# Optimization experiments

Measured on AMD Instinct MI355X. Metric: run time of the kernel, lower is better.

## Reference

```python
import jax, jax.numpy as jnp
import numpy as np

PRED_STEPS = 5
NEG = 16
C = 256
B = 64
H = 16
W = 16
SKIP = 1
EPS = 1e-11


def setup_inputs() -> dict:
    key = jax.random.key(0)
    ks = jax.random.split(key, 3 + PRED_STEPS)
    inp = {
        "z": jax.random.normal(ks[0], (B, C, H, W), jnp.float32),
        "c": jax.random.normal(ks[1], (B, C, H, W), jnp.float32),
        "Wk": jax.random.normal(ks[2], (PRED_STEPS, C, C), jnp.float32) * 0.05,
    }
    for k in range(1, PRED_STEPS + 1):
        rows = (H - k - SKIP) * W * B
        inp[f"rand_idx_{k}"] = jax.random.randint(ks[2 + k], (rows * NEG,), 0, rows, dtype=jnp.int64 if jax.config.jax_enable_x64 else jnp.int32)
    return inp


def reference(z, c, Wk, rand_idx_1, rand_idx_2, rand_idx_3, rand_idx_4, rand_idx_5):
    idx_list = [rand_idx_1, rand_idx_2, rand_idx_3, rand_idx_4, rand_idx_5]
    total_loss = jnp.float32(0.0)
    patchwise_loss = jnp.zeros((B, H, W), jnp.float32)
    patchwise_count = jnp.zeros((H, W), jnp.float32)
    for k in range(1, PRED_STEPS + 1):
        off = k + SKIP
        Hk = H - off
        # 1x1 conv projection, permuted to [Hk, W, B, C]
        ztwk = jnp.einsum('oi,bihw->hwbo', Wk[k - 1], z[:, :, off:, :])
        # random-gather negatives: [Hk, W, B, NEG, C]
        flat = ztwk.reshape(Hk * W * B, C)
        ztwk_shuf = flat[idx_list[k - 1]].reshape(Hk, W, B, NEG, C)
        # context: [Hk, W, B, C]
        ctx = jnp.transpose(c[:, :, :Hk, :], (2, 3, 0, 1))
        # scoring
        main = jnp.einsum('hwbc,hwbc->hwb', ctx, ztwk)[..., None]        # [Hk,W,B,1]
        negs = jnp.einsum('hwbc,hwbnc->hwbn', ctx, ztwk_shuf)            # [Hk,W,B,NEG]
        logits = jnp.concatenate([main, negs], axis=-1)                  # [Hk,W,B,1+NEG]
        log_fk = jnp.transpose(logits, (2, 3, 0, 1))                     # [B,1+NEG,Hk,W]
        sm = jax.nn.softmax(log_fk, axis=1)
        stu_loss = -jnp.log(sm[:, 0, :, :] + EPS)                        # [B,Hk,W]
        total_loss = total_loss + stu_loss.mean()
        patchwise_loss = patchwise_loss.at[:, off:, :].add(stu_loss)
        patchwise_loss = patchwise_loss.at[:, :H - off, :].add(stu_loss)
        ones = jnp.ones((Hk, W), jnp.float32)
        patchwise_count = patchwise_count.at[off:, :].add(ones)
        patchwise_count = patchwise_count.at[:H - off, :].add(ones)
    total_loss = total_loss / PRED_STEPS
    return (total_loss, patchwise_loss, patchwise_count)
```

## Files before the change

kernel.cpp:

```cpp
#include <hip/hip_runtime.h>
#include <hip/hip_bf16.h>
#include <math.h>

#define NEG_ 16
#define PRED_ 5
#define EPS_ 1e-11f
#define LDW 18
#define GSTR 272
#define ASTR 72

typedef __attribute__((ext_vector_type(8))) short bf16x8;
typedef __attribute__((ext_vector_type(4))) float f32x4;

static __device__ __forceinline__ unsigned short f2bu(float f) {
  __hip_bfloat16 h = __float2bfloat16(f);
  return *(unsigned short*)&h;
}


__global__ __launch_bounds__(256) void prep_all(
    const float* __restrict__ z, const float* __restrict__ c,
    const float* __restrict__ Wk,
    unsigned short* __restrict__ Zp, unsigned short* __restrict__ Cb,
    unsigned short* __restrict__ Wb) {
  __shared__ float tile[32][33];
  int tx = threadIdx.x, ty = threadIdx.y;
  if (blockIdx.y == 7) {
    if (blockIdx.z == 0 && blockIdx.x < 320) {
      int i = blockIdx.x * 256 + ty * 32 + tx;
      float4 v = ((const float4*)Wk)[i];
      ushort4 o;
      o.x = f2bu(v.x); o.y = f2bu(v.y); o.z = f2bu(v.z); o.w = f2bu(v.w);
      ((ushort4*)Wb)[i] = o;
    }
    return;
  }
  const float* in = blockIdx.z ? c : z;
  unsigned short* out = blockIdx.z ? Cb : Zp;
  int p0 = blockIdx.x * 32;
  int q0 = blockIdx.y * 32 + (blockIdx.z ? 0 : 32);
#pragma unroll
  for (int r = 0; r < 32; r += 8)
    tile[ty + r][tx] = in[(size_t)(p0 + ty + r) * 256 + q0 + tx];
  __syncthreads();
#pragma unroll
  for (int r = 0; r < 32; r += 8)
    out[(size_t)(q0 + ty + r) * 16384 + p0 + tx] = f2bu(tile[tx][ty + r]);
}

__global__ __launch_bounds__(256) void gemm_all(
    const unsigned short* __restrict__ Zp, const unsigned short* __restrict__ Wb,
    unsigned short* __restrict__ Yb) {
  const int kk = blockIdx.z;
  const int Mk = (14 - kk) * 1024;
  const int m0b = blockIdx.y * 128;
  if (m0b >= Mk) return;
  const unsigned short* A = Zp + (size_t)(kk + 2) * 1024 * 256;
  const unsigned short* Wm = Wb + (size_t)kk * 65536;
  unsigned short* Y = Yb + (size_t)kk * 14336 * 256;
  __shared__ unsigned short As[128 * ASTR];
  __shared__ unsigned short Bs[128 * ASTR];
  const int t = threadIdx.x;
  const int wid = t >> 6, lane = t & 63;
  const int wm = wid >> 1, wn = wid & 1;
  const int l15 = lane & 15, quad = lane >> 4;
  const int n0 = blockIdx.x * 128;
  const int srow = t >> 1, shalf = t & 1;
  const unsigned short* ga = A + (size_t)(m0b + srow) * 256 + shalf * 32;
  const unsigned short* gb = Wm + (size_t)(n0 + srow) * 256 + shalf * 32;
  unsigned short* wa = As + srow * ASTR + shalf * 32;
  unsigned short* wb = Bs + srow * ASTR + shalf * 32;
  f32x4 acc[4][4] = {};
  bf16x8 ra[4], rb[4];
#pragma unroll
  for (int cs = 0; cs < 4; ++cs) {
    ra[cs] = *(const bf16x8*)(ga + cs * 8);
    rb[cs] = *(const bf16x8*)(gb + cs * 8);
  }
#pragma unroll
  for (int ki = 0; ki < 4; ++ki) {
    __syncthreads();
#pragma unroll
    for (int cs = 0; cs < 4; ++cs) {
      *(bf16x8*)(wa + cs * 8) = ra[cs];
      *(bf16x8*)(wb + cs * 8) = rb[cs];
    }
    __syncthreads();
    if (ki < 3) {
      const int k1 = (ki + 1) * 64;
#pragma unroll
      for (int cs = 0; cs < 4; ++cs) {
        ra[cs] = *(const bf16x8*)(ga + k1 + cs * 8);
        rb[cs] = *(const bf16x8*)(gb + k1 + cs * 8);
      }
    }
#pragma unroll
    for (int ks = 0; ks < 2; ++ks) {
      bf16x8 af[4], bf[4];
#pragma unroll
      for (int tm = 0; tm < 4; ++tm)
        af[tm] = *(const bf16x8*)(As + (wm * 64 + tm * 16 + l15) * ASTR + ks * 32 + quad * 8);
#pragma unroll
      for (int tn = 0; tn < 4; ++tn)
        bf[tn] = *(const bf16x8*)(Bs + (wn * 64 + tn * 16 + l15) * ASTR + ks * 32 + quad * 8);
#pragma unroll
      for (int tm = 0; tm < 4; ++tm)
#pragma unroll
        for (int tn = 0; tn < 4; ++tn)
          acc[tm][tn] = __builtin_amdgcn_mfma_f32_16x16x32_bf16(
              af[tm], bf[tn], acc[tm][tn], 0, 0, 0);
    }
  }
#pragma unroll
  for (int tm = 0; tm < 4; ++tm)
#pragma unroll
    for (int tn = 0; tn < 4; ++tn)
#pragma unroll
      for (int r = 0; r < 4; ++r)
        Y[(size_t)(m0b + wm * 64 + tm * 16 + quad * 4 + r) * 256 +
          n0 + wn * 64 + tn * 16 + l15] = f2bu(acc[tm][tn][r]);
}

__global__ __launch_bounds__(256) void score_all(
    const unsigned short* __restrict__ Yb, const unsigned short* __restrict__ Cb,
    const int* __restrict__ r1, const int* __restrict__ r2,
    const int* __restrict__ r3, const int* __restrict__ r4,
    const int* __restrict__ r5, float* __restrict__ Lk) {
  __shared__ __align__(16) unsigned short gbuf[4][16 * GSTR];
  __shared__ float L[16 * LDW];
  const int wv = threadIdx.x >> 6, lane = threadIdx.x & 63;
  const int gid = blockIdx.x;
  int kk, base;
  if (gid < 896)       { kk = 0; base = 0; }
  else if (gid < 1728) { kk = 1; base = 896; }
  else if (gid < 2496) { kk = 2; base = 1728; }
  else if (gid < 3200) { kk = 3; base = 2496; }
  else                 { kk = 4; base = 3200; }
  const int Mk = (14 - kk) * 1024;
  const int m0 = (gid - base) * 16;
  const int* ridx = kk == 0 ? r1 : kk == 1 ? r2 : kk == 2 ? r3 : kk == 3 ? r4 : r5;
  const unsigned short* Y = Yb + (size_t)kk * 14336 * 256;
  const int l15 = lane & 15, quad = lane >> 4;
  const int half = lane >> 5, ch = lane & 31;
  unsigned short* mybuf = gbuf[wv];

  auto gather = [&](const unsigned short* src, int iv, bf16x8* dst) {
#pragma unroll
    for (int j = 0; j < 8; ++j) {
      int rlo = __shfl(iv, 2 * j);
      int rhi = __shfl(iv, 2 * j + 1);
      int row = half ? rhi : rlo;
      dst[j] = *(const bf16x8*)(src + (size_t)row * 256 + ch * 8);
    }
  };
  auto stage = [&](const bf16x8* g) {
#pragma unroll
    for (int j2 = 0; j2 < 8; ++j2)
      *(bf16x8*)(mybuf + (2 * j2 + half) * GSTR + ch * 8) = g[j2];
  };

  bf16x8 af[8];
  {
    bf16x8 g[8];
    gather(Cb, m0 + l15, g);
    stage(g);
#pragma unroll
    for (int tv = 0; tv < 8; ++tv)
      af[tv] = *(const bf16x8*)(mybuf + l15 * GSTR + quad * 8 + tv * 32);
  }

  const int c0 = (wv == 0) ? 0 : (4 * wv + 1);
  const int nc = (wv == 0) ? 5 : 4;
  auto load_iv = [&](int c) -> int {
    if (c == 0) return m0 + l15;
    int idx = ridx[(m0 + (c - 1)) * NEG_ + l15];
    return idx < 0 ? 0 : (idx >= Mk ? Mk - 1 : idx);
  };

  bf16x8 g[8], gn[8];
  gather(Y, load_iv(c0), g);
  for (int j = 0; j < nc; ++j) {
    if (j + 1 < nc) gather(Y, load_iv(c0 + j + 1), gn);
    stage(g);
    f32x4 acc = {};
#pragma unroll
    for (int tv = 0; tv < 8; ++tv) {
      bf16x8 bf = *(const bf16x8*)(mybuf + l15 * GSTR + quad * 8 + tv * 32);
      acc = __builtin_amdgcn_mfma_f32_16x16x32_bf16(af[tv], bf, acc, 0, 0, 0);
    }
    const int c = c0 + j;
    if (c == 0) {
#pragma unroll
      for (int r = 0; r < 4; ++r)
        if (l15 == quad * 4 + r) L[(quad * 4 + r) * LDW] = acc[r];
    } else {
      const int i = c - 1;
      if (quad == (i >> 2)) L[i * LDW + 1 + l15] = acc[i & 3];
    }
#pragma unroll
    for (int tv = 0; tv < 8; ++tv) g[tv] = gn[tv];
  }
  __syncthreads();
  if (threadIdx.x < 16) {
    float mainv = L[threadIdx.x * LDW];
    float mx = mainv;
    float nv[NEG_];
#pragma unroll
    for (int n = 0; n < NEG_; ++n) {
      nv[n] = L[threadIdx.x * LDW + 1 + n];
      mx = fmaxf(mx, nv[n]);
    }
    float num = __expf(mainv - mx);
    float se = num;
#pragma unroll
    for (int n = 0; n < NEG_; ++n) se += __expf(nv[n] - mx);
    Lk[kk * 14336 + m0 + threadIdx.x] = -logf(num / se + EPS_);
  }
}

__global__ __launch_bounds__(256) void finalize_pl(
    const float* __restrict__ Lk, float* __restrict__ out) {
  if (blockIdx.x < 64) {
    int idx = blockIdx.x * 256 + threadIdx.x;
    int b = idx >> 8, h = (idx >> 4) & 15, w = idx & 15;
    float v = 0.f;
#pragma unroll
    for (int kk = 0; kk < PRED_; ++kk) {
      int off = kk + 2;
      if (h >= off)      v += Lk[kk * 14336 + ((h - off) * 16 + w) * 64 + b];
      if (h <= 15 - off) v += Lk[kk * 14336 + (h * 16 + w) * 64 + b];
    }
    out[1 + idx] = v;
    if (idx < 256) {
      int hh = idx >> 4;
      float cnt = 0.f;
#pragma unroll
      for (int off = 2; off <= 6; ++off)
        cnt += (hh >= off ? 1.f : 0.f) + (hh <= 15 - off ? 1.f : 0.f);
      out[1 + 16384 + idx] = cnt;
    }
  } else {
    __shared__ float red[256];
    const int t = threadIdx.x;
    float local = 0.f;
#pragma unroll
    for (int kk = 0; kk < PRED_; ++kk) {
      const int Mk = (14 - kk) * 1024;
      const float scale = 1.0f / (5120.0f * (float)(14 - kk));
      for (int e = t; e < Mk; e += 256)
        local += Lk[kk * 14336 + e] * scale;
    }
    red[t] = local;
    __syncthreads();
    for (int s = 128; s; s >>= 1) {
      if (t < s) red[t] += red[t + s];
      __syncthreads();
    }
    if (t == 0) out[0] = red[0];
  }
}

extern "C" void kernel_launch(void* const* d_in, const int* in_sizes, int n_in,
                              void* d_out, int out_size, void* d_ws, size_t ws_size,
                              hipStream_t stream) {
  const float* z  = (const float*)d_in[0];
  const float* c  = (const float*)d_in[1];
  const float* Wk = (const float*)d_in[2];
  float* out = (float*)d_out;
  char* wsb = (char*)d_ws;
  unsigned short* Zp = (unsigned short*)(wsb);
  unsigned short* Cb = (unsigned short*)(wsb + 8388608);
  unsigned short* Wb = (unsigned short*)(wsb + 16777216);
  unsigned short* Yb = (unsigned short*)(wsb + 17432576);
  float*          Lk = (float*)(wsb + 54132736);

  prep_all<<<dim3(512, 8, 2), dim3(32, 8), 0, stream>>>(z, c, Wk, Zp, Cb, Wb);
  gemm_all<<<dim3(2, 112, PRED_), 256, 0, stream>>>(Zp, Wb, Yb);
  score_all<<<3840, 256, 0, stream>>>(
      Yb, Cb, (const int*)d_in[3], (const int*)d_in[4], (const int*)d_in[5],
      (const int*)d_in[6], (const int*)d_in[7], Lk);
  finalize_pl<<<65, 256, 0, stream>>>(Lk, out);
}
```

Baseline: 185.5 us.

## Deepen gather prefetch to two stages and widen the prep transpose tile

In the scoring kernel, the single-step register double buffer for row gathers becomes a three-slot ring, so two gathers are in flight ahead of the MFMA work and the per-iteration register copy goes away. The prep transpose now uses a 64x32 tile with a flat 256-thread block. Each output row is written as 64 contiguous bf16 values, and Wk conversion work is spread across both z slices. The cost is more live registers, and the ring slot chosen by j%3 inside a loop with a runtime trip count may force the compiler to spill to scratch.

```diff
diff --git a/kernel.cpp b/kernel.cpp
--- a/kernel.cpp
+++ b/kernel.cpp
@@ -23,11 +23,12 @@
     const float* __restrict__ Wk,
     unsigned short* __restrict__ Zp, unsigned short* __restrict__ Cb,
     unsigned short* __restrict__ Wb) {
-  __shared__ float tile[32][33];
-  int tx = threadIdx.x, ty = threadIdx.y;
+  __shared__ float tile[32][65];
+  const int t = threadIdx.x;
   if (blockIdx.y == 7) {
-    if (blockIdx.z == 0 && blockIdx.x < 320) {
-      int i = blockIdx.x * 256 + ty * 32 + tx;
+    int ib = blockIdx.z * 256 + blockIdx.x;
+    if (ib < 320) {
+      int i = ib * 256 + t;
       float4 v = ((const float4*)Wk)[i];
       ushort4 o;
       o.x = f2bu(v.x); o.y = f2bu(v.y); o.z = f2bu(v.z); o.w = f2bu(v.w);
@@ -37,15 +38,17 @@
   }
   const float* in = blockIdx.z ? c : z;
   unsigned short* out = blockIdx.z ? Cb : Zp;
-  int p0 = blockIdx.x * 32;
-  int q0 = blockIdx.y * 32 + (blockIdx.z ? 0 : 32);
-#pragma unroll
-  for (int r = 0; r < 32; r += 8)
-    tile[ty + r][tx] = in[(size_t)(p0 + ty + r) * 256 + q0 + tx];
+  const int p0 = blockIdx.x * 64;
+  const int q0 = blockIdx.y * 32 + (blockIdx.z ? 0 : 32);
+  const int tx = t & 31, ty = t >> 5;
+#pragma unroll
+  for (int r = 0; r < 64; r += 8)
+    tile[tx][ty + r] = in[(size_t)(p0 + ty + r) * 256 + q0 + tx];
   __syncthreads();
-#pragma unroll
-  for (int r = 0; r < 32; r += 8)
-    out[(size_t)(q0 + ty + r) * 16384 + p0 + tx] = f2bu(tile[tx][ty + r]);
+  const int pp = t & 63, wq = t >> 6;
+#pragma unroll
+  for (int r = 0; r < 32; r += 4)
+    out[(size_t)(q0 + wq + r) * 16384 + p0 + pp] = f2bu(tile[wq + r][pp]);
 }
 
 __global__ __launch_bounds__(256) void gemm_all(
@@ -177,11 +180,12 @@
     return idx < 0 ? 0 : (idx >= Mk ? Mk - 1 : idx);
   };
 
-  bf16x8 g[8], gn[8];
-  gather(Y, load_iv(c0), g);
+  bf16x8 ring[3][8];
+  gather(Y, load_iv(c0), ring[0]);
+  gather(Y, load_iv(c0 + 1), ring[1]);
   for (int j = 0; j < nc; ++j) {
-    if (j + 1 < nc) gather(Y, load_iv(c0 + j + 1), gn);
-    stage(g);
+    if (j + 2 < nc) gather(Y, load_iv(c0 + j + 2), ring[(j + 2) % 3]);
+    stage(ring[j % 3]);
     f32x4 acc = {};
 #pragma unroll
     for (int tv = 0; tv < 8; ++tv) {
@@ -197,8 +201,6 @@
       const int i = c - 1;
       if (quad == (i >> 2)) L[i * LDW + 1 + l15] = acc[i & 3];
     }
-#pragma unroll
-    for (int tv = 0; tv < 8; ++tv) g[tv] = gn[tv];
   }
   __syncthreads();
   if (threadIdx.x < 16) {
@@ -274,7 +276,7 @@
   unsigned short* Yb = (unsigned short*)(wsb + 17432576);
   float*          Lk = (float*)(wsb + 54132736);
 
-  prep_all<<<dim3(512, 8, 2), dim3(32, 8), 0, stream>>>(z, c, Wk, Zp, Cb, Wb);
+  prep_all<<<dim3(256, 8, 2), 256, 0, stream>>>(z, c, Wk, Zp, Cb, Wb);
   gemm_all<<<dim3(2, 112, PRED_), 256, 0, stream>>>(Zp, Wb, Yb);
   score_all<<<3840, 256, 0, stream>>>(
       Yb, Cb, (const int*)d_in[3], (const int*)d_in[4], (const int*)d_in[5],
```

Result: slower. 347.8 us (+87.5%).
